# Performance work log

Hardware: AMD Instinct MI355X
Metric: run time of the kernel (lower is better)

Reference implementation:

```python
import jax, jax.numpy as jnp
import numpy as np

ALPHA = 0.2  # LeakyReLU negative slope

def setup_inputs() -> dict:
    key = jax.random.key(0)
    k1, k2, k3 = jax.random.split(key, 3)
    N, F_in, F_out = 8192, 128, 64
    h = jax.random.normal(k1, (N, F_in), dtype=jnp.float32)
    W = jax.random.normal(k2, (F_in, F_out), dtype=jnp.float32) * 0.1
    a = jax.random.normal(k3, (2 * F_out, 1), dtype=jnp.float32) * 0.1
    return {"h": h, "W": W, "a": a}

def reference(h, W, a):
    # Wh: [N, F_out]
    Wh = h @ W
    F_out = Wh.shape[1]
    # Split 'a' into source/dest halves; e_ij = leakyrelu(a1.Wh_i + a2.Wh_j)
    a1 = a[:F_out, 0]   # [F_out]
    a2 = a[F_out:, 0]   # [F_out]
    e_src = Wh @ a1     # [N]
    e_dst = Wh @ a2     # [N]
    e = e_src[:, None] + e_dst[None, :]          # [N, N]
    e = jnp.where(e > 0, e, ALPHA * e)           # leaky relu
    attention = jax.nn.softmax(e, axis=1)        # dropout omitted (eval mode)
    h_prime = attention @ Wh                     # [N, F_out]
    return jax.nn.elu(h_prime)                   # concat=True path
```

## Files before the change

### kernel.cpp

```cpp
#include <hip/hip_runtime.h>


typedef unsigned long long ull;

constexpr int N_ROWS = 8192;
constexpr int F_IN   = 128;
constexpr int F_OUT  = 64;
#define LRELU_ALPHA 0.2f

constexpr int SBLK = 8;
constexpr int NGRP = N_ROWS / SBLK;

constexpr int WS_WH   = 0;
constexpr int WS_ESRC = WS_WH + N_ROWS * F_OUT;
constexpr int WS_KEYA = WS_ESRC + N_ROWS;
constexpr int WS_KEYB = WS_KEYA + 2 * N_ROWS;
constexpr int WS_GS1T = WS_KEYB + 2 * N_ROWS;
constexpr int WS_GS2T = WS_GS1T + F_OUT * NGRP;
constexpr int WS_GD1  = WS_GS2T + F_OUT * NGRP;
constexpr int WS_GD2  = WS_GD1 + NGRP;
constexpr int WS_P1   = WS_GD2 + NGRP;
constexpr int WS_P2   = WS_P1 + (NGRP + 1) * F_OUT;
constexpr int WS_D1   = WS_P2 + (NGRP + 1) * F_OUT;
constexpr int WS_D2   = WS_D1 + (NGRP + 1);
static_assert((WS_KEYA % 2) == 0 && (WS_KEYB % 2) == 0, "keys 8B-aligned");

__device__ __forceinline__ unsigned mono_enc(float f) {
  unsigned u = __float_as_uint(f);
  return u ^ ((u & 0x80000000u) ? 0xFFFFFFFFu : 0x80000000u);
}
__device__ __forceinline__ float mono_dec(unsigned e) {
  unsigned u = e ^ ((e & 0x80000000u) ? 0x80000000u : 0xFFFFFFFFu);
  return __uint_as_float(u);
}

__global__ __launch_bounds__(256) void k1_wh(const float* __restrict__ h,
                                             const float* __restrict__ W,
                                             const float* __restrict__ a,
                                             float* __restrict__ ws) {
  __shared__ float hlds[16 * F_IN];
  __shared__ float alds[2 * F_OUT];
  const int t = threadIdx.x;
  const int row0 = blockIdx.x * 16;

  const float4* hsrc = (const float4*)(h + (long)row0 * F_IN);
  float4* hd = (float4*)hlds;
  hd[t]       = hsrc[t];
  hd[t + 256] = hsrc[t + 256];
  if (t < 2 * F_OUT) alds[t] = a[t];
  __syncthreads();

  const int wave = t >> 6, lane = t & 63;
  const float* hp = hlds + (wave * 4) * F_IN;
  float acc0 = 0.f, acc1 = 0.f, acc2 = 0.f, acc3 = 0.f;

  #pragma unroll 4
  for (int k4 = 0; k4 < F_IN; k4 += 4) {
    float4 h0 = *(const float4*)(hp + k4);
    float4 h1 = *(const float4*)(hp + F_IN + k4);
    float4 h2 = *(const float4*)(hp + 2 * F_IN + k4);
    float4 h3 = *(const float4*)(hp + 3 * F_IN + k4);
    float w0 = W[(k4 + 0) * F_OUT + lane];
    float w1 = W[(k4 + 1) * F_OUT + lane];
    float w2 = W[(k4 + 2) * F_OUT + lane];
    float w3 = W[(k4 + 3) * F_OUT + lane];
    acc0 = fmaf(h0.x, w0, acc0); acc0 = fmaf(h0.y, w1, acc0);
    acc0 = fmaf(h0.z, w2, acc0); acc0 = fmaf(h0.w, w3, acc0);
    acc1 = fmaf(h1.x, w0, acc1); acc1 = fmaf(h1.y, w1, acc1);
    acc1 = fmaf(h1.z, w2, acc1); acc1 = fmaf(h1.w, w3, acc1);
    acc2 = fmaf(h2.x, w0, acc2); acc2 = fmaf(h2.y, w1, acc2);
    acc2 = fmaf(h2.z, w2, acc2); acc2 = fmaf(h2.w, w3, acc2);
    acc3 = fmaf(h3.x, w0, acc3); acc3 = fmaf(h3.y, w1, acc3);
    acc3 = fmaf(h3.z, w2, acc3); acc3 = fmaf(h3.w, w3, acc3);
  }

  const int grow = row0 + wave * 4;
  float* Wh = ws + WS_WH;
  Wh[(grow + 0) * F_OUT + lane] = acc0;
  Wh[(grow + 1) * F_OUT + lane] = acc1;
  Wh[(grow + 2) * F_OUT + lane] = acc2;
  Wh[(grow + 3) * F_OUT + lane] = acc3;

  const float a1 = alds[lane], a2 = alds[F_OUT + lane];
  float s0 = acc0 * a1, s1 = acc1 * a1, s2 = acc2 * a1, s3 = acc3 * a1;
  float d0 = acc0 * a2, d1 = acc1 * a2, d2 = acc2 * a2, d3 = acc3 * a2;
  #pragma unroll
  for (int off = 32; off; off >>= 1) {
    s0 += __shfl_down(s0, off); s1 += __shfl_down(s1, off);
    s2 += __shfl_down(s2, off); s3 += __shfl_down(s3, off);
    d0 += __shfl_down(d0, off); d1 += __shfl_down(d1, off);
    d2 += __shfl_down(d2, off); d3 += __shfl_down(d3, off);
  }
  if (lane == 0) {
    ws[WS_ESRC + grow + 0] = s0; ws[WS_ESRC + grow + 1] = s1;
    ws[WS_ESRC + grow + 2] = s2; ws[WS_ESRC + grow + 3] = s3;
    ull* keys = (ull*)(ws + WS_KEYA);
    keys[grow + 0] = ((ull)mono_enc(d0) << 32) | (unsigned)(grow + 0);
    keys[grow + 1] = ((ull)mono_enc(d1) << 32) | (unsigned)(grow + 1);
    keys[grow + 2] = ((ull)mono_enc(d2) << 32) | (unsigned)(grow + 2);
    keys[grow + 3] = ((ull)mono_enc(d3) << 32) | (unsigned)(grow + 3);
  }
}

__global__ __launch_bounds__(1024) void k2a_1024(ull* __restrict__ keys) {
  __shared__ ull lk[1024];
  const int t = threadIdx.x;
  const int base = blockIdx.x * 1024;
  lk[t] = keys[base + t];
  __syncthreads();
  for (int k = 2; k <= 1024; k <<= 1) {
    for (int j = k >> 1; j > 0; j >>= 1) {
      int p = t ^ j;
      if (p > t) {
        ull x = lk[t], y = lk[p];
        bool asc = ((t & k) == 0);
        if ((x > y) == asc) { lk[t] = y; lk[p] = x; }
      }
      __syncthreads();
    }
  }
  keys[base + t] = lk[t];
}

template <int RUN>
__global__ __launch_bounds__(256) void k_merge(const ull* __restrict__ src,
                                               ull* __restrict__ dst) {
  const int g = blockIdx.x * 256 + threadIdx.x;
  const ull key = src[g];
  const int pairbase = g & ~(2 * RUN - 1);
  const int local = g - pairbase;
  const bool inA = local < RUN;
  const ull* other = src + pairbase + (inA ? RUN : 0);
  const int idx = inA ? local : (local - RUN);
  int lo = 0, hi = RUN;
  while (lo < hi) {
    int m = (lo + hi) >> 1;
    if (other[m] < key) lo = m + 1; else hi = m;
  }
  dst[pairbase + idx + lo] = key;
}

__global__ __launch_bounds__(256) void k3a_gs(float* __restrict__ ws) {
  const int t = threadIdx.x, wv = t >> 6, lane = t & 63;
  const int g = blockIdx.x * 4 + wv;
  const ull* K = (const ull*)(ws + WS_KEYB);
  const float* Wh = ws + WS_WH;
  float s1 = 0.f, s2 = 0.f, sd1 = 0.f, sd2 = 0.f;
  #pragma unroll
  for (int o = 0; o < SBLK; ++o) {
    ull key = K[(g << 3) + o];
    float d = mono_dec((unsigned)(key >> 32));
    int j = (int)(key & 0xFFFFFFFFu);
    float e1 = __expf(d), e2 = __expf(LRELU_ALPHA * d);
    float v = Wh[j * F_OUT + lane];
    s1 = fmaf(e1, v, s1); s2 = fmaf(e2, v, s2);
    sd1 += e1; sd2 += e2;
  }
  ws[WS_GS1T + lane * NGRP + g] = s1;
  ws[WS_GS2T + lane * NGRP + g] = s2;
  if (lane == 0) { ws[WS_GD1 + g] = sd1; ws[WS_GD2 + g] = sd2; }
}

__global__ __launch_bounds__(1024) void k3b_scan(float* __restrict__ ws) {
  __shared__ float sm[1024];
  const int t = threadIdx.x;
  const int blk = blockIdx.x;
  const float* src;
  int c = 0;
  if (blk < 64)        { c = blk;      src = ws + WS_GS1T + c * NGRP; }
  else if (blk < 128)  { c = blk - 64; src = ws + WS_GS2T + c * NGRP; }
  else if (blk == 128) { src = ws + WS_GD1; }
  else                 { src = ws + WS_GD2; }

  const float x = src[t];
  sm[t] = x;
  __syncthreads();
  for (int off = 1; off < 1024; off <<= 1) {
    float y = (t >= off) ? sm[t - off] : 0.f;
    __syncthreads();
    sm[t] += y;
    __syncthreads();
  }
  const float incl = sm[t];
  const float excl = incl - x;
  if (blk < 64) {
    ws[WS_P1 + t * F_OUT + c] = excl;
    if (t == NGRP - 1) ws[WS_P1 + NGRP * F_OUT + c] = incl;
  } else if (blk < 128) {
    ws[WS_P2 + t * F_OUT + c] = excl;
    if (t == NGRP - 1) ws[WS_P2 + NGRP * F_OUT + c] = incl;
  } else if (blk == 128) {
    ws[WS_D1 + t] = excl;
    if (t == NGRP - 1) ws[WS_D1 + NGRP] = incl;
  } else {
    ws[WS_D2 + t] = excl;
    if (t == NGRP - 1) ws[WS_D2 + NGRP] = incl;
  }
}

__global__ __launch_bounds__(256) void k4_out(const float* __restrict__ ws,
                                              float* __restrict__ out) {
  const int t = threadIdx.x, wv = t >> 6, lane = t & 63;
  const int i = blockIdx.x * 4 + wv;
  const ull* K = (const ull*)(ws + WS_KEYB);
  const float s = ws[WS_ESRC + i];
  const float ns = (s == 0.0f) ? 0.0f : -s;
  const unsigned Ki = mono_enc(ns);

  unsigned m1 = (unsigned)(K[lane << 7] >> 32);
  ull bal1 = __ballot(m1 <= Ki);
  int tl;
  if (bal1 == 0ull) {
    tl = 0;
  } else {
    int L1 = 63 - __clzll((long long)bal1);
    int base = L1 << 7;
    unsigned m2 = (unsigned)(K[base + (lane << 1)] >> 32);
    ull bal2 = __ballot(m2 <= Ki);
    int L2 = 63 - __clzll((long long)bal2);
    int p = base + (L2 << 1) + 1;
    unsigned m3 = (unsigned)(K[p] >> 32);
    tl = p + ((m3 <= Ki) ? 1 : 0);
  }
  const int b = tl >> 3, rr = tl & 7;

  float p1 = ws[WS_P1 + b * F_OUT + lane];
  float p2 = ws[WS_P2 + b * F_OUT + lane];
  float d1 = ws[WS_D1 + b], d2 = ws[WS_D2 + b];
  const float p1tot = ws[WS_P1 + NGRP * F_OUT + lane];
  const float d1tot = ws[WS_D1 + NGRP];
  const float* Wh = ws + WS_WH;

  for (int o = 0; o < rr; ++o) {
    ull key = K[(b << 3) + o];
    float d = mono_dec((unsigned)(key >> 32));
    int j = (int)(key & 0xFFFFFFFFu);
    float e1 = __expf(d), e2 = __expf(LRELU_ALPHA * d);
    float v = Wh[j * F_OUT + lane];
    p1 = fmaf(e1, v, p1); p2 = fmaf(e2, v, p2);
    d1 += e1; d2 += e2;
  }

  const float es1 = __expf(s), es2 = __expf(LRELU_ALPHA * s);
  const float num = es1 * (p1tot - p1) + es2 * p2;
  const float den = es1 * (d1tot - d1) + es2 * d2;
  const float r = num / den;
  out[i * F_OUT + lane] = (r > 0.f) ? r : (__expf(r) - 1.f);
}

extern "C" void kernel_launch(void* const* d_in, const int* in_sizes, int n_in,
                              void* d_out, int out_size, void* d_ws, size_t ws_size,
                              hipStream_t stream) {
  const float* h = (const float*)d_in[0];
  const float* W = (const float*)d_in[1];
  const float* a = (const float*)d_in[2];
  float* ws = (float*)d_ws;
  float* out = (float*)d_out;
  ull* keyA = (ull*)(ws + WS_KEYA);
  ull* keyB = (ull*)(ws + WS_KEYB);

  hipLaunchKernelGGL(k1_wh,         dim3(N_ROWS / 16), dim3(256),  0, stream, h, W, a, ws);
  hipLaunchKernelGGL(k2a_1024,      dim3(8),           dim3(1024), 0, stream, keyA);
  hipLaunchKernelGGL(k_merge<1024>, dim3(32),          dim3(256),  0, stream, keyA, keyB);
  hipLaunchKernelGGL(k_merge<2048>, dim3(32),          dim3(256),  0, stream, keyB, keyA);
  hipLaunchKernelGGL(k_merge<4096>, dim3(32),          dim3(256),  0, stream, keyA, keyB);
  hipLaunchKernelGGL(k3a_gs,        dim3(NGRP / 4),    dim3(256),  0, stream, ws);
  hipLaunchKernelGGL(k3b_scan,      dim3(130),         dim3(1024), 0, stream, ws);
  hipLaunchKernelGGL(k4_out,        dim3(N_ROWS / 4),  dim3(256),  0, stream, ws, out);
}
```

Before: 102.0 us.

## Replace merge passes with single rank kernel and fuse group-sum with scan

Three separate merge-pass launches are replaced with one kernel. It loads all 8192 sorted-run keys into shared memory (64KB) and computes each key's final position by binary-searching the other seven runs. The per-group weighted sums and the prefix scans are merged into a single 65-block kernel that scans two arrays together, so the GS1T/GS2T intermediate tables are no longer written and re-read. This cuts the launch count from 8 to 5. In exchange, each rank block does seven binary searches per key, and the fused table kernel reads Wh with a strided, per-column access pattern.

```diff
diff --git a/kernel.cpp b/kernel.cpp
--- a/kernel.cpp
+++ b/kernel.cpp
@@ -122,79 +122,92 @@
   keys[base + t] = lk[t];
 }
 
-template <int RUN>
-__global__ __launch_bounds__(256) void k_merge(const ull* __restrict__ src,
+__global__ __launch_bounds__(512) void k2_rank(const ull* __restrict__ src,
                                                ull* __restrict__ dst) {
-  const int g = blockIdx.x * 256 + threadIdx.x;
-  const ull key = src[g];
-  const int pairbase = g & ~(2 * RUN - 1);
-  const int local = g - pairbase;
-  const bool inA = local < RUN;
-  const ull* other = src + pairbase + (inA ? RUN : 0);
-  const int idx = inA ? local : (local - RUN);
-  int lo = 0, hi = RUN;
-  while (lo < hi) {
-    int m = (lo + hi) >> 1;
-    if (other[m] < key) lo = m + 1; else hi = m;
-  }
-  dst[pairbase + idx + lo] = key;
-}
-
-__global__ __launch_bounds__(256) void k3a_gs(float* __restrict__ ws) {
-  const int t = threadIdx.x, wv = t >> 6, lane = t & 63;
-  const int g = blockIdx.x * 4 + wv;
+  __shared__ ull lk[8192];
+  const int t = threadIdx.x;
+  #pragma unroll
+  for (int c = 0; c < 16; ++c) lk[c * 512 + t] = src[c * 512 + t];
+  __syncthreads();
+
+  const int g = blockIdx.x * 512 + t;
+  const ull key = lk[g];
+  const int myrun = g >> 10;
+  int pos = g & 1023;
+
+  #pragma unroll
+  for (int r = 0; r < 8; ++r) {
+    if (r == myrun) continue;
+    const ull* base = lk + (r << 10);
+    int p = 0;
+    #pragma unroll
+    for (int step = 512; step >= 1; step >>= 1)
+      p += (base[p + step - 1] < key) ? step : 0;
+    p += (base[p] < key) ? 1 : 0;
+    pos += p;
+  }
+  dst[pos] = key;
+}
+
+__global__ __launch_bounds__(1024) void k3_tables(float* __restrict__ ws) {
+  __shared__ float sa[1024];
+  __shared__ float sb[1024];
+  const int t = threadIdx.x;
+  const int blk = blockIdx.x;
   const ull* K = (const ull*)(ws + WS_KEYB);
   const float* Wh = ws + WS_WH;
-  float s1 = 0.f, s2 = 0.f, sd1 = 0.f, sd2 = 0.f;
-  #pragma unroll
-  for (int o = 0; o < SBLK; ++o) {
-    ull key = K[(g << 3) + o];
-    float d = mono_dec((unsigned)(key >> 32));
-    int j = (int)(key & 0xFFFFFFFFu);
-    float e1 = __expf(d), e2 = __expf(LRELU_ALPHA * d);
-    float v = Wh[j * F_OUT + lane];
-    s1 = fmaf(e1, v, s1); s2 = fmaf(e2, v, s2);
-    sd1 += e1; sd2 += e2;
-  }
-  ws[WS_GS1T + lane * NGRP + g] = s1;
-  ws[WS_GS2T + lane * NGRP + g] = s2;
-  if (lane == 0) { ws[WS_GD1 + g] = sd1; ws[WS_GD2 + g] = sd2; }
-}
-
-__global__ __launch_bounds__(1024) void k3b_scan(float* __restrict__ ws) {
-  __shared__ float sm[1024];
-  const int t = threadIdx.x;
-  const int blk = blockIdx.x;
-  const float* src;
-  int c = 0;
-  if (blk < 64)        { c = blk;      src = ws + WS_GS1T + c * NGRP; }
-  else if (blk < 128)  { c = blk - 64; src = ws + WS_GS2T + c * NGRP; }
-  else if (blk == 128) { src = ws + WS_GD1; }
-  else                 { src = ws + WS_GD2; }
-
-  const float x = src[t];
-  sm[t] = x;
+
+  float s1 = 0.f, s2 = 0.f;
+  if (blk < 64) {
+    const int c = blk;
+    const ull* kp = K + (t << 3);
+    #pragma unroll
+    for (int o = 0; o < SBLK; ++o) {
+      ull key = kp[o];
+      float d = mono_dec((unsigned)(key >> 32));
+      int j = (int)(key & 0xFFFFFFFFu);
+      float e1 = __expf(d), e2 = __expf(LRELU_ALPHA * d);
+      float v = Wh[j * F_OUT + c];
+      s1 = fmaf(e1, v, s1); s2 = fmaf(e2, v, s2);
+    }
+  } else {
+    const ull* kp = K + (t << 3);
+    #pragma unroll
+    for (int o = 0; o < SBLK; ++o) {
+      ull key = kp[o];
+      float d = mono_dec((unsigned)(key >> 32));
+      s1 += __expf(d); s2 += __expf(LRELU_ALPHA * d);
+    }
+  }
+
+  const float xa = s1, xb = s2;
+  sa[t] = xa; sb[t] = xb;
   __syncthreads();
   for (int off = 1; off < 1024; off <<= 1) {
-    float y = (t >= off) ? sm[t - off] : 0.f;
+    float ya = (t >= off) ? sa[t - off] : 0.f;
+    float yb = (t >= off) ? sb[t - off] : 0.f;
     __syncthreads();
-    sm[t] += y;
+    sa[t] += ya; sb[t] += yb;
     __syncthreads();
   }
-  const float incl = sm[t];
-  const float excl = incl - x;
+  const float ia = sa[t], ib = sb[t];
+  const float ea = ia - xa, eb = ib - xb;
+
   if (blk < 64) {
-    ws[WS_P1 + t * F_OUT + c] = excl;
-    if (t == NGRP - 1) ws[WS_P1 + NGRP * F_OUT + c] = incl;
-  } else if (blk < 128) {
-    ws[WS_P2 + t * F_OUT + c] = excl;
-    if (t == NGRP - 1) ws[WS_P2 + NGRP * F_OUT + c] = incl;
-  } else if (blk == 128) {
-    ws[WS_D1 + t] = excl;
-    if (t == NGRP - 1) ws[WS_D1 + NGRP] = incl;
+    const int c = blk;
+    ws[WS_P1 + t * F_OUT + c] = ea;
+    ws[WS_P2 + t * F_OUT + c] = eb;
+    if (t == NGRP - 1) {
+      ws[WS_P1 + NGRP * F_OUT + c] = ia;
+      ws[WS_P2 + NGRP * F_OUT + c] = ib;
+    }
   } else {
-    ws[WS_D2 + t] = excl;
-    if (t == NGRP - 1) ws[WS_D2 + NGRP] = incl;
+    ws[WS_D1 + t] = ea;
+    ws[WS_D2 + t] = eb;
+    if (t == NGRP - 1) {
+      ws[WS_D1 + NGRP] = ia;
+      ws[WS_D2 + NGRP] = ib;
+    }
   }
 }
 
@@ -259,12 +272,9 @@
   ull* keyA = (ull*)(ws + WS_KEYA);
   ull* keyB = (ull*)(ws + WS_KEYB);
 
-  hipLaunchKernelGGL(k1_wh,         dim3(N_ROWS / 16), dim3(256),  0, stream, h, W, a, ws);
-  hipLaunchKernelGGL(k2a_1024,      dim3(8),           dim3(1024), 0, stream, keyA);
-  hipLaunchKernelGGL(k_merge<1024>, dim3(32),          dim3(256),  0, stream, keyA, keyB);
-  hipLaunchKernelGGL(k_merge<2048>, dim3(32),          dim3(256),  0, stream, keyB, keyA);
-  hipLaunchKernelGGL(k_merge<4096>, dim3(32),          dim3(256),  0, stream, keyA, keyB);
-  hipLaunchKernelGGL(k3a_gs,        dim3(NGRP / 4),    dim3(256),  0, stream, ws);
-  hipLaunchKernelGGL(k3b_scan,      dim3(130),         dim3(1024), 0, stream, ws);
-  hipLaunchKernelGGL(k4_out,        dim3(N_ROWS / 4),  dim3(256),  0, stream, ws, out);
-}
+  hipLaunchKernelGGL(k1_wh,     dim3(N_ROWS / 16), dim3(256),  0, stream, h, W, a, ws);
+  hipLaunchKernelGGL(k2a_1024,  dim3(8),           dim3(1024), 0, stream, keyA);
+  hipLaunchKernelGGL(k2_rank,   dim3(16),          dim3(512),  0, stream, keyA, keyB);
+  hipLaunchKernelGGL(k3_tables, dim3(65),          dim3(1024), 0, stream, ws);
+  hipLaunchKernelGGL(k4_out,    dim3(N_ROWS / 4),  dim3(256),  0, stream, ws, out);
+}
```

After: 99.69 us. 2.3% less time.
